# Optimization experiments

Measured on AMD Instinct MI355X. Metric: run time of the kernel, lower is better.

## Reference

```python
import jax, jax.numpy as jnp
import numpy as np

DIM, HEADS, PAIR_DIM = 256, 8, 128
B, S, N = 1, 128, 256
DH = DIM // HEADS
SCALE = DH ** -0.5
EPS = 1e-5


def setup_inputs() -> dict:
    key = jax.random.key(0)
    ks = jax.random.split(key, 12)
    s = lambda fan_in: 1.0 / np.sqrt(fan_in)
    return {
        "msa": jax.random.normal(ks[0], (B, S, N, DIM), jnp.float32),
        "pair": jax.random.normal(ks[1], (B, N, N, PAIR_DIM), jnp.float32),
        "mask": jax.random.randint(ks[2], (B, N, N), 0, 2, jnp.int32),
        "Wqkv": jax.random.normal(ks[3], (3 * DIM, DIM), jnp.float32) * s(DIM),
        "bqkv": jnp.zeros((3 * DIM,), jnp.float32),
        "Wout": jax.random.normal(ks[4], (DIM, DIM), jnp.float32) * s(DIM),
        "bout": jnp.zeros((DIM,), jnp.float32),
        "Wpb": jax.random.normal(ks[5], (HEADS, PAIR_DIM), jnp.float32) * s(PAIR_DIM),
        "bpb": jnp.zeros((HEADS,), jnp.float32),
        "gamma": jnp.ones((DIM,), jnp.float32),
        "beta": jnp.zeros((DIM,), jnp.float32),
    }


def reference(msa, pair, mask, Wqkv, bqkv, Wout, bout, Wpb, bpb, gamma, beta):
    # qkv projection: [B,S,N,3*DIM] -> [B,S,N,3,H,DH]
    qkv = (msa @ Wqkv.T + bqkv).reshape(B, S, N, 3, HEADS, DH)
    q, k, v = qkv[..., 0, :, :], qkv[..., 1, :, :], qkv[..., 2, :, :]
    # scores [B,S,H,N,N]
    attn = jnp.einsum('bsnhc,bsmhc->bshnm', q, k) * SCALE
    attn = jnp.where(mask[:, None, None, :, :] == 0, -1e9, attn)
    # pair bias: [B,N,N,P] -> [B,1,H,N,N]
    pair_bias = (pair @ Wpb.T + bpb).transpose(0, 3, 1, 2)[:, None]
    attn = jax.nn.softmax(attn + pair_bias, axis=-1)
    out = jnp.einsum('bshnm,bsmhc->bsnhc', attn, v).reshape(B, S, N, DIM)
    out = out @ Wout.T + bout
    # residual + layernorm
    x = msa + out
    mu = jnp.mean(x, axis=-1, keepdims=True)
    var = jnp.var(x, axis=-1, keepdims=True)
    return (x - mu) * jax.lax.rsqrt(var + EPS) * gamma + beta
```

## Files before the change

### kernel.cpp

```cpp
#include <hip/hip_runtime.h>
#include <cstdint>
#include <cstddef>

typedef unsigned short u16;
typedef __bf16 bf16x8 __attribute__((ext_vector_type(8)));
typedef float f32x4 __attribute__((ext_vector_type(4)));
typedef unsigned int u32x4 __attribute__((ext_vector_type(4)));

#define SCALE_QK_LOG2 0.25509904f
#define INV_LN2 1.4426950408889634f

__device__ __forceinline__ u16 f2bf(float f){ return __builtin_bit_cast(u16, (__bf16)f); }
__device__ __forceinline__ float bf2f(u16 u){ unsigned v = ((unsigned)u)<<16; return __builtin_bit_cast(float, v); }
__device__ __forceinline__ bf16x8 ldfrag_g(const u16* p){
  return __builtin_bit_cast(bf16x8, *reinterpret_cast<const u32x4*>(p));
}
__device__ __forceinline__ void gload16(const u16* g, u16* lds){
  __builtin_amdgcn_global_load_lds((const __attribute__((address_space(1))) unsigned int*)g,
                                   (__attribute__((address_space(3))) unsigned int*)lds, 16, 0, 0);
}

__global__ __launch_bounds__(256) void k_cvt(const float* __restrict__ src,
                                             u16* __restrict__ dst, int n4){
  int stride = gridDim.x * blockDim.x;
  for (int idx = blockIdx.x*blockDim.x + threadIdx.x; idx < n4; idx += stride){
    float4 v = reinterpret_cast<const float4*>(src)[idx];
    ushort4 o;
    o.x = f2bf(v.x); o.y = f2bf(v.y); o.z = f2bf(v.z); o.w = f2bf(v.w);
    reinterpret_cast<ushort4*>(dst)[idx] = o;
  }
}

__global__ __launch_bounds__(256) void k_cvt2(const float* __restrict__ a, u16* __restrict__ da,
                                              const float* __restrict__ b, u16* __restrict__ db){
  int bid = blockIdx.x;
  if (bid < 192){
    int idx = bid*256 + threadIdx.x;
    float4 v = reinterpret_cast<const float4*>(a)[idx];
    ushort4 o; o.x=f2bf(v.x); o.y=f2bf(v.y); o.z=f2bf(v.z); o.w=f2bf(v.w);
    reinterpret_cast<ushort4*>(da)[idx] = o;
  } else {
    int idx = (bid-192)*256 + threadIdx.x;
    float4 v = reinterpret_cast<const float4*>(b)[idx];
    ushort4 o; o.x=f2bf(v.x); o.y=f2bf(v.y); o.z=f2bf(v.z); o.w=f2bf(v.w);
    reinterpret_cast<ushort4*>(db)[idx] = o;
  }
}

__global__ __launch_bounds__(256) void k_pair_bias(const float* __restrict__ pair,
        const int* __restrict__ mask, const float* __restrict__ Wpb,
        const float* __restrict__ bpb, u16* __restrict__ bT){
  __shared__ float wsm[8][128];
  __shared__ float bsm[8];
  int tid = threadIdx.x;
  for (int i = tid; i < 1024; i += 256) wsm[i>>7][i&127] = Wpb[i];
  if (tid < 8) bsm[tid] = bpb[tid];
  __syncthreads();
  int g = tid>>4, l = tid&15;
  int row = blockIdx.x*16 + g;
  const float4* p = reinterpret_cast<const float4*>(pair + (size_t)row*128);
  float4 a0 = p[l];
  float4 a1 = p[l+16];
  int c0 = 4*l, c1 = 64 + 4*l;
  float acc[8];
#pragma unroll
  for (int hh=0; hh<8; hh++){
    acc[hh] = a0.x*wsm[hh][c0] + a0.y*wsm[hh][c0+1] + a0.z*wsm[hh][c0+2] + a0.w*wsm[hh][c0+3]
            + a1.x*wsm[hh][c1] + a1.y*wsm[hh][c1+1] + a1.z*wsm[hh][c1+2] + a1.w*wsm[hh][c1+3];
  }
#pragma unroll
  for (int hh=0; hh<8; hh++){
    float v = acc[hh];
    v += __shfl_xor(v,1); v += __shfl_xor(v,2); v += __shfl_xor(v,4); v += __shfl_xor(v,8);
    acc[hh] = v;
  }
  if (l == 0){
    float mb = (mask[row] == 0) ? -1e9f : 0.0f;
    int n = row>>8, m = row&255;
#pragma unroll
    for (int hh=0; hh<8; hh++)
      bT[hh*65536 + m*256 + n] = f2bf((acc[hh] + bsm[hh] + mb) * INV_LN2);
  }
}

__global__ __launch_bounds__(256, 3) void k_qkv(const u16* __restrict__ A,
                                                const u16* __restrict__ B,
                                                const float* __restrict__ bq,
                                                u16* __restrict__ qkv){
  __shared__ __align__(16) u16 Al[128*64];
  __shared__ __align__(16) u16 Bl[128*64];
  const int tid = threadIdx.x;
  const int w = tid>>6, l = tid&63;
  const int wm = w>>1, wn = w&1;
  const int m0 = blockIdx.y*128, n0 = blockIdx.x*128;
  const int lr = l&15, lg = l>>4;
  f32x4 acc[4][4] = {};
  for (int kt=0; kt<4; ++kt){
    const int k0 = kt*64;
    __syncthreads();
#pragma unroll
    for (int j=0;j<4;j++){
      int ch = w*256 + j*64 + l;
      int r = ch>>3, sl = ch&7;
      gload16(A + (size_t)(m0+r)*256 + k0 + ((sl^(r&7))*8), Al + (size_t)(w*256 + j*64)*8);
      gload16(B + (size_t)(n0+r)*256 + k0 + ((sl^(r&7))*8), Bl + (size_t)(w*256 + j*64)*8);
    }
    __syncthreads();
#pragma unroll
    for (int ks=0; ks<2; ++ks){
      bf16x8 af[4], bfr[4];
#pragma unroll
      for (int t=0;t<4;t++){
        int ra = wm*64 + t*16 + lr;
        int sa = (ks*4 + lg) ^ (ra&7);
        af[t] = __builtin_bit_cast(bf16x8, *reinterpret_cast<const u32x4*>(&Al[ra*64 + sa*8]));
        int rb = wn*64 + t*16 + lr;
        int sb = (ks*4 + lg) ^ (rb&7);
        bfr[t] = __builtin_bit_cast(bf16x8, *reinterpret_cast<const u32x4*>(&Bl[rb*64 + sb*8]));
      }
#pragma unroll
      for (int tm=0;tm<4;tm++)
#pragma unroll
        for (int tn=0;tn<4;tn++)
          acc[tm][tn] = __builtin_amdgcn_mfma_f32_16x16x32_bf16(af[tm], bfr[tn], acc[tm][tn], 0,0,0);
    }
  }
#pragma unroll
  for (int tn=0;tn<4;tn++){
    int c = n0 + wn*64 + tn*16 + lr;
    int t3 = c>>8, hh = (c>>5)&7, dh = c&31;
    float bb = bq[c];
    u16* obase = qkv + (size_t)(t3*8+hh)*32768*32 + dh;
#pragma unroll
    for (int tm=0;tm<4;tm++){
#pragma unroll
      for (int rr=0;rr<4;rr++){
        int m = m0 + wm*64 + tm*16 + lg*4 + rr;
        obase[(size_t)m*32] = f2bf(acc[tm][tn][rr] + bb);
      }
    }
  }
}

__global__ __launch_bounds__(256, 2) void k_attn(const u16* __restrict__ qkv,
                                                 const u16* __restrict__ bT,
                                                 u16* __restrict__ O){
  __shared__ __align__(16) u16 vT[32*256];
  __shared__ __align__(16) u16 P[4][32*64];
  const int h = blockIdx.x, s = blockIdx.y, z = blockIdx.z;
  const int tid = threadIdx.x;
  const int w = tid>>6, l = tid&63;
  const int lr = l&15, lg = l>>4;
  const int n0 = z*128 + 32*w;
  const u16* qb = qkv + ((size_t)h*32768 + s*256)*32;
  const u16* kb = qkv + ((size_t)(8+h)*32768 + s*256)*32;
  const u16* vb = qkv + ((size_t)(16+h)*32768 + s*256)*32;
  const u16* bb = bT + h*65536;

#pragma unroll
  for (int i=0;i<4;i++){
    int flat4 = tid + 256*i;
    int m = flat4>>2, d0 = (flat4&3)*8;
    u32x4 d = *reinterpret_cast<const u32x4*>(vb + (size_t)m*32 + d0);
    u16 tmp[8];
    *reinterpret_cast<u32x4*>(tmp) = d;
#pragma unroll
    for (int j=0;j<8;j++){
      int dh = d0 + j;
      vT[dh*256 + (((m>>3)^(dh&7))*8) + (m&7)] = tmp[j];
    }
  }
  __syncthreads();

  bf16x8 qf[2];
#pragma unroll
  for (int t=0;t<2;t++)
    qf[t] = ldfrag_g(qb + (size_t)(n0 + t*16 + lr)*32 + lg*8);

  f32x4 sacc[2][16] = {};
#pragma unroll
  for (int kt=0; kt<4; ++kt){
    bf16x8 kf[4];
#pragma unroll
    for (int tn=0;tn<4;tn++)
      kf[tn] = ldfrag_g(kb + (size_t)(kt*64 + tn*16 + lr)*32 + lg*8);
#pragma unroll
    for (int t=0;t<2;t++)
#pragma unroll
      for (int tn=0;tn<4;tn++)
        sacc[t][kt*4+tn] = __builtin_amdgcn_mfma_f32_16x16x32_bf16(qf[t], kf[tn], sacc[t][kt*4+tn], 0,0,0);
  }

#pragma unroll
  for (int kt=0;kt<4;kt++){
#pragma unroll
    for (int t=0;t<2;t++)
#pragma unroll
      for (int tn=0;tn<4;tn++){
        ushort4 b4 = *reinterpret_cast<const ushort4*>(
            bb + (size_t)(kt*64 + tn*16 + lr)*256 + n0 + t*16 + lg*4);
        float bc[4] = { bf2f(b4.x), bf2f(b4.y), bf2f(b4.z), bf2f(b4.w) };
#pragma unroll
        for (int rr=0;rr<4;rr++)
          sacc[t][kt*4+tn][rr] = sacc[t][kt*4+tn][rr]*SCALE_QK_LOG2 + bc[rr];
      }
  }

  float inv_l[2][4];
#pragma unroll
  for (int t=0;t<2;t++){
#pragma unroll
    for (int rr=0;rr<4;rr++){
      float mx = sacc[t][0][rr];
#pragma unroll
      for (int j=1;j<16;j++) mx = fmaxf(mx, sacc[t][j][rr]);
      mx = fmaxf(mx, __shfl_xor(mx,1));
      mx = fmaxf(mx, __shfl_xor(mx,2));
      mx = fmaxf(mx, __shfl_xor(mx,4));
      mx = fmaxf(mx, __shfl_xor(mx,8));
      float ps = 0.f;
#pragma unroll
      for (int j=0;j<16;j++){
        float p = __builtin_amdgcn_exp2f(sacc[t][j][rr] - mx);
        sacc[t][j][rr] = p;
        ps += p;
      }
      ps += __shfl_xor(ps,1);
      ps += __shfl_xor(ps,2);
      ps += __shfl_xor(ps,4);
      ps += __shfl_xor(ps,8);
      inv_l[t][rr] = 1.0f / ps;
    }
  }

  f32x4 oacc[2][2] = {};
#pragma unroll
  for (int mt=0; mt<4; ++mt){
#pragma unroll
    for (int t=0;t<2;t++){
#pragma unroll
      for (int rr=0;rr<4;rr++){
        int row = t*16 + lg*4 + rr;
        int rb = row*64;
        int sx = row&7;
#pragma unroll
        for (int tn=0;tn<4;tn++){
          int col = tn*16 + lr;
          P[w][rb + (((col>>3)^sx)*8) + (col&7)] = f2bf(sacc[t][mt*4+tn][rr]);
        }
      }
    }
#pragma unroll
    for (int kk=0;kk<2;kk++){
      bf16x8 vf[2];
#pragma unroll
      for (int dt=0;dt<2;dt++){
        int c = dt*16 + lr;
        int slot = (mt*8 + kk*4 + lg) ^ (c&7);
        vf[dt] = __builtin_bit_cast(bf16x8, *reinterpret_cast<const u32x4*>(&vT[c*256 + slot*8]));
      }
#pragma unroll
      for (int t=0;t<2;t++){
        int ra = t*16 + lr;
        int sa = (kk*4 + lg) ^ (ra&7);
        bf16x8 pf = __builtin_bit_cast(bf16x8, *reinterpret_cast<const u32x4*>(&P[w][ra*64 + sa*8]));
        oacc[t][0] = __builtin_amdgcn_mfma_f32_16x16x32_bf16(pf, vf[0], oacc[t][0], 0,0,0);
        oacc[t][1] = __builtin_amdgcn_mfma_f32_16x16x32_bf16(pf, vf[1], oacc[t][1], 0,0,0);
      }
    }
  }
#pragma unroll
  for (int t=0;t<2;t++){
#pragma unroll
    for (int rr=0;rr<4;rr++){
      int n = n0 + t*16 + lg*4 + rr;
      float inv = inv_l[t][rr];
      size_t rowb = (size_t)(s*256 + n)*256 + h*32;
#pragma unroll
      for (int dt=0;dt<2;dt++)
        O[rowb + dt*16 + lr] = f2bf(oacc[t][dt][rr]*inv);
    }
  }
}

__global__ __launch_bounds__(256, 3) void k_out_ln(const u16* __restrict__ A,
        const u16* __restrict__ Wo, const float* __restrict__ bo,
        const float* __restrict__ msa, const float* __restrict__ gamma,
        const float* __restrict__ beta, float* __restrict__ out){
  __shared__ __align__(16) u16 Al[64*64];
  __shared__ __align__(16) u16 Wl[256*64];
  __shared__ float redS[64][4];
  __shared__ float redQ[64][4];
  const int tid = threadIdx.x;
  const int w = tid>>6, l = tid&63;
  const int lr = l&15, lg = l>>4;
  const int m0 = blockIdx.x*64;
  f32x4 acc[4][4] = {};
  for (int kt=0;kt<4;kt++){
    const int k0 = kt*64;
    __syncthreads();
#pragma unroll
    for (int j=0;j<2;j++){
      int ch = w*128 + j*64 + l;
      int r = ch>>3, sl = ch&7;
      gload16(A + (size_t)(m0+r)*256 + k0 + ((sl^(r&7))*8), Al + (size_t)(w*128 + j*64)*8);
    }
#pragma unroll
    for (int j=0;j<8;j++){
      int ch = w*512 + j*64 + l;
      int r = ch>>3, sl = ch&7;
      gload16(Wo + (size_t)r*256 + k0 + ((sl^(r&7))*8), Wl + (size_t)(w*512 + j*64)*8);
    }
    __syncthreads();
#pragma unroll
    for (int ks=0;ks<2;ks++){
      bf16x8 af[4], bfr[4];
#pragma unroll
      for (int t=0;t<4;t++){
        int ra = t*16 + lr;
        int sa = (ks*4+lg) ^ (ra&7);
        af[t] = __builtin_bit_cast(bf16x8, *reinterpret_cast<const u32x4*>(&Al[ra*64 + sa*8]));
        int rb = w*64 + t*16 + lr;
        int sb = (ks*4+lg) ^ (rb&7);
        bfr[t] = __builtin_bit_cast(bf16x8, *reinterpret_cast<const u32x4*>(&Wl[rb*64 + sb*8]));
      }
#pragma unroll
      for (int tm=0;tm<4;tm++)
#pragma unroll
        for (int tn=0;tn<4;tn++)
          acc[tm][tn] = __builtin_amdgcn_mfma_f32_16x16x32_bf16(af[tm], bfr[tn], acc[tm][tn], 0,0,0);
    }
  }
#pragma unroll
  for (int tn=0;tn<4;tn++){
    int c = w*64 + tn*16 + lr;
    float bc = bo[c];
#pragma unroll
    for (int tm=0;tm<4;tm++)
#pragma unroll
      for (int rr=0;rr<4;rr++){
        int m = m0 + tm*16 + lg*4 + rr;
        acc[tm][tn][rr] += bc + msa[(size_t)m*256 + c];
      }
  }
#pragma unroll
  for (int tm=0;tm<4;tm++){
#pragma unroll
    for (int rr=0;rr<4;rr++){
      float sS = 0.f, sQ = 0.f;
#pragma unroll
      for (int tn=0;tn<4;tn++){
        float v = acc[tm][tn][rr];
        sS += v; sQ += v*v;
      }
      sS += __shfl_xor(sS,1); sS += __shfl_xor(sS,2); sS += __shfl_xor(sS,4); sS += __shfl_xor(sS,8);
      sQ += __shfl_xor(sQ,1); sQ += __shfl_xor(sQ,2); sQ += __shfl_xor(sQ,4); sQ += __shfl_xor(sQ,8);
      if (lr == 0){
        int row = tm*16 + lg*4 + rr;
        redS[row][w] = sS;
        redQ[row][w] = sQ;
      }
    }
  }
  __syncthreads();
#pragma unroll
  for (int tm=0;tm<4;tm++){
#pragma unroll
    for (int rr=0;rr<4;rr++){
      int row = tm*16 + lg*4 + rr;
      float S = redS[row][0]+redS[row][1]+redS[row][2]+redS[row][3];
      float Q = redQ[row][0]+redQ[row][1]+redQ[row][2]+redQ[row][3];
      float mu = S * (1.0f/256.0f);
      float var = Q * (1.0f/256.0f) - mu*mu;
      float inv = rsqrtf(var + 1e-5f);
      int m = m0 + row;
#pragma unroll
      for (int tn=0;tn<4;tn++){
        int c = w*64 + tn*16 + lr;
        out[(size_t)m*256 + c] = (acc[tm][tn][rr]-mu)*inv*gamma[c] + beta[c];
      }
    }
  }
}

extern "C" void kernel_launch(void* const* d_in, const int* in_sizes, int n_in,
                              void* d_out, int out_size, void* d_ws, size_t ws_size,
                              hipStream_t stream) {
  const float* msa  = (const float*)d_in[0];
  const float* pair = (const float*)d_in[1];
  const int*   mask = (const int*)d_in[2];
  const float* Wqkv = (const float*)d_in[3];
  const float* bqkv = (const float*)d_in[4];
  const float* Wout = (const float*)d_in[5];
  const float* bout = (const float*)d_in[6];
  const float* Wpb  = (const float*)d_in[7];
  const float* bpb  = (const float*)d_in[8];
  const float* gamma= (const float*)d_in[9];
  const float* beta = (const float*)d_in[10];
  float* out = (float*)d_out;

  char* ws = (char*)d_ws;
  u16*   msa_bf  = (u16*)(ws);
  u16*   wqkv_bf = (u16*)(ws + 16777216);
  u16*   wout_bf = (u16*)(ws + 17170432);
  u16*   biasT   = (u16*)(ws + 17301504);
  u16*   qkvb    = (u16*)(ws + 18350080);
  u16*   Ob      = (u16*)(ws + 68681728);

  k_cvt<<<4096, 256, 0, stream>>>(msa, msa_bf, 8388608/4);
  k_cvt2<<<256, 256, 0, stream>>>(Wqkv, wqkv_bf, Wout, wout_bf);
  k_pair_bias<<<4096, 256, 0, stream>>>(pair, mask, Wpb, bpb, biasT);
  k_qkv<<<dim3(6,256), 256, 0, stream>>>(msa_bf, wqkv_bf, bqkv, qkvb);
  k_attn<<<dim3(8,128,2), 256, 0, stream>>>(qkvb, biasT, Ob);
  k_out_ln<<<512, 256, 0, stream>>>(Ob, wout_bf, bout, msa, gamma, beta, out);
}
```

Measured before the change: 233.4 us.

## Write V transposed from QKV GEMM and read V fragments from global in attention

```diff
diff --git a/kernel.cpp b/kernel.cpp
--- a/kernel.cpp
+++ b/kernel.cpp
@@ -86,7 +86,8 @@
 __global__ __launch_bounds__(256, 3) void k_qkv(const u16* __restrict__ A,
                                                 const u16* __restrict__ B,
                                                 const float* __restrict__ bq,
-                                                u16* __restrict__ qkv){
+                                                u16* __restrict__ qkv,
+                                                u16* __restrict__ vTg){
   __shared__ __align__(16) u16 Al[128*64];
   __shared__ __align__(16) u16 Bl[128*64];
   const int tid = threadIdx.x;
@@ -130,22 +131,33 @@
     int c = n0 + wn*64 + tn*16 + lr;
     int t3 = c>>8, hh = (c>>5)&7, dh = c&31;
     float bb = bq[c];
-    u16* obase = qkv + (size_t)(t3*8+hh)*32768*32 + dh;
-#pragma unroll
-    for (int tm=0;tm<4;tm++){
-#pragma unroll
-      for (int rr=0;rr<4;rr++){
-        int m = m0 + wm*64 + tm*16 + lg*4 + rr;
-        obase[(size_t)m*32] = f2bf(acc[tm][tn][rr] + bb);
-      }
-    }
-  }
-}
-
-__global__ __launch_bounds__(256, 2) void k_attn(const u16* __restrict__ qkv,
+    if (t3 < 2){
+      u16* obase = qkv + (size_t)(t3*8+hh)*32768*32 + dh;
+#pragma unroll
+      for (int tm=0;tm<4;tm++)
+#pragma unroll
+        for (int rr=0;rr<4;rr++){
+          int m = m0 + wm*64 + tm*16 + lg*4 + rr;
+          obase[(size_t)m*32] = f2bf(acc[tm][tn][rr] + bb);
+        }
+    } else {
+      u16* vbase = vTg + ((size_t)hh*128*32 + dh)*256;
+#pragma unroll
+      for (int tm=0;tm<4;tm++)
+#pragma unroll
+        for (int rr=0;rr<4;rr++){
+          int m = m0 + wm*64 + tm*16 + lg*4 + rr;
+          int s = m>>8, key = m&255;
+          vbase[(size_t)s*32*256 + key] = f2bf(acc[tm][tn][rr] + bb);
+        }
+    }
+  }
+}
+
+__global__ __launch_bounds__(256, 3) void k_attn(const u16* __restrict__ qkv,
+                                                 const u16* __restrict__ vTg,
                                                  const u16* __restrict__ bT,
                                                  u16* __restrict__ O){
-  __shared__ __align__(16) u16 vT[32*256];
   __shared__ __align__(16) u16 P[4][32*64];
   const int h = blockIdx.x, s = blockIdx.y, z = blockIdx.z;
   const int tid = threadIdx.x;
@@ -154,23 +166,8 @@
   const int n0 = z*128 + 32*w;
   const u16* qb = qkv + ((size_t)h*32768 + s*256)*32;
   const u16* kb = qkv + ((size_t)(8+h)*32768 + s*256)*32;
-  const u16* vb = qkv + ((size_t)(16+h)*32768 + s*256)*32;
+  const u16* vg = vTg + ((size_t)(h*128 + s)*32)*256;
   const u16* bb = bT + h*65536;
-
-#pragma unroll
-  for (int i=0;i<4;i++){
-    int flat4 = tid + 256*i;
-    int m = flat4>>2, d0 = (flat4&3)*8;
-    u32x4 d = *reinterpret_cast<const u32x4*>(vb + (size_t)m*32 + d0);
-    u16 tmp[8];
-    *reinterpret_cast<u32x4*>(tmp) = d;
-#pragma unroll
-    for (int j=0;j<8;j++){
-      int dh = d0 + j;
-      vT[dh*256 + (((m>>3)^(dh&7))*8) + (m&7)] = tmp[j];
-    }
-  }
-  __syncthreads();
 
   bf16x8 qf[2];
 #pragma unroll
@@ -256,8 +253,7 @@
 #pragma unroll
       for (int dt=0;dt<2;dt++){
         int c = dt*16 + lr;
-        int slot = (mt*8 + kk*4 + lg) ^ (c&7);
-        vf[dt] = __builtin_bit_cast(bf16x8, *reinterpret_cast<const u32x4*>(&vT[c*256 + slot*8]));
+        vf[dt] = ldfrag_g(vg + (size_t)c*256 + mt*64 + kk*32 + lg*8);
       }
 #pragma unroll
       for (int t=0;t<2;t++){
@@ -405,12 +401,13 @@
   u16*   wout_bf = (u16*)(ws + 17170432);
   u16*   biasT   = (u16*)(ws + 17301504);
   u16*   qkvb    = (u16*)(ws + 18350080);
+  u16*   vTg     = (u16*)(ws + 51904512);
   u16*   Ob      = (u16*)(ws + 68681728);
 
   k_cvt<<<4096, 256, 0, stream>>>(msa, msa_bf, 8388608/4);
   k_cvt2<<<256, 256, 0, stream>>>(Wqkv, wqkv_bf, Wout, wout_bf);
   k_pair_bias<<<4096, 256, 0, stream>>>(pair, mask, Wpb, bpb, biasT);
-  k_qkv<<<dim3(6,256), 256, 0, stream>>>(msa_bf, wqkv_bf, bqkv, qkvb);
-  k_attn<<<dim3(8,128,2), 256, 0, stream>>>(qkvb, biasT, Ob);
+  k_qkv<<<dim3(6,256), 256, 0, stream>>>(msa_bf, wqkv_bf, bqkv, qkvb, vTg);
+  k_attn<<<dim3(8,128,2), 256, 0, stream>>>(qkvb, vTg, biasT, Ob);
   k_out_ln<<<512, 256, 0, stream>>>(Ob, wout_bf, bout, msa, gamma, beta, out);
 }
```

New measurement: 267.2 us. 1.14x slower.
